# Optimization experiments

Hardware: AMD Instinct MI355X
Metric: run time of the kernel (lower is better)

## Reference

```python
import jax, jax.numpy as jnp
import numpy as np

DIM = 32
N_HOP = 2
N_MEMORY = 32
BATCH = 2048
N_ENTITY = 100000
N_RELATION = 48


def _gru_cell(x, h, w_ih, w_hh, b_ih, b_hh):
    # PyTorch GRUCell semantics
    gi = x @ w_ih.T + b_ih          # [b, 3d]
    gh = h @ w_hh.T + b_hh          # [b, 3d]
    i_r, i_z, i_n = jnp.split(gi, 3, axis=-1)
    h_r, h_z, h_n = jnp.split(gh, 3, axis=-1)
    r = jax.nn.sigmoid(i_r + h_r)
    z = jax.nn.sigmoid(i_z + h_z)
    n = jnp.tanh(i_n + r * h_n)
    return (1.0 - z) * n + z * h


def setup_inputs() -> dict:
    key = jax.random.key(0)
    ks = jax.random.split(key, 16)
    h_i = jax.random.randint(ks[0], (BATCH, N_HOP, N_MEMORY), 0, N_ENTITY)
    R_i = jax.random.randint(ks[1], (BATCH, N_HOP, N_MEMORY), 0, N_RELATION)
    t_i = jax.random.randint(ks[2], (BATCH, N_HOP, N_MEMORY), 0, N_ENTITY)
    v_i = jax.random.randint(ks[3], (BATCH,), 0, N_ENTITY)
    s = 0.05
    entity_emb = jax.random.normal(ks[4], (N_ENTITY, DIM), jnp.float32) * s
    relation_emb = jax.random.normal(ks[5], (N_RELATION, DIM, DIM), jnp.float32) * s
    agg_w1 = jax.random.normal(ks[6], (DIM, 4 * DIM), jnp.float32) * s
    agg_b1 = jnp.zeros((DIM,), jnp.float32)
    agg_w2 = jax.random.normal(ks[7], (1, DIM), jnp.float32) * s
    agg_b2 = jnp.zeros((1,), jnp.float32)
    gru_w_ih = jax.random.normal(ks[8], (N_HOP, 3 * DIM, DIM), jnp.float32) * s
    gru_w_hh = jax.random.normal(ks[9], (N_HOP, 3 * DIM, DIM), jnp.float32) * s
    gru_b_ih = jnp.zeros((N_HOP, 3 * DIM), jnp.float32)
    gru_b_hh = jnp.zeros((N_HOP, 3 * DIM), jnp.float32)
    ans_w = jax.random.normal(ks[10], (DIM, DIM), jnp.float32) * s
    ans_b = jnp.zeros((DIM,), jnp.float32)
    return {
        'h_i': h_i, 'R_i': R_i, 't_i': t_i, 'v_i': v_i,
        'entity_emb': entity_emb, 'relation_emb': relation_emb,
        'agg_w1': agg_w1, 'agg_b1': agg_b1, 'agg_w2': agg_w2, 'agg_b2': agg_b2,
        'gru_w_ih': gru_w_ih, 'gru_w_hh': gru_w_hh,
        'gru_b_ih': gru_b_ih, 'gru_b_hh': gru_b_hh,
        'ans_w': ans_w, 'ans_b': ans_b,
    }


def reference(h_i, R_i, t_i, v_i, entity_emb, relation_emb,
              agg_w1, agg_b1, agg_w2, agg_b2,
              gru_w_ih, gru_w_hh, gru_b_ih, gru_b_hh,
              ans_w, ans_b):
    # InputModule: embedding gathers
    vs = entity_emb[v_i]                     # [b, d]
    hs = entity_emb[h_i]                     # [b, H, m, d]
    ts = entity_emb[t_i]                     # [b, H, m, d]
    Rs = relation_emb[R_i]                   # [b, H, m, d, d]

    M = vs
    n_hop = hs.shape[1]
    for hop in range(n_hop):
        R = Rs[:, hop]                       # [b, m, d, d]
        h = hs[:, hop]                       # [b, m, d]
        t = ts[:, hop]                       # [b, m, d]
        Rh = jnp.einsum('bmij,bmj->bmi', R, h)   # [b, m, d]
        vexp = vs[:, None, :]
        mexp = M[:, None, :]
        z = jnp.concatenate([Rh * vexp, Rh * mexp,
                             jnp.abs(Rh - vexp), jnp.abs(Rh - mexp)], axis=2)  # [b, m, 4d]
        # AggregateFnc: tanh(Linear) -> Linear(d,1); dropout is eval-mode identity
        Z = jnp.tanh(z @ agg_w1.T + agg_b1) @ agg_w2.T + agg_b2   # [b, m, 1]
        g = jax.nn.softmax(Z[..., 0], axis=1)[..., None]           # [b, m, 1]
        o = jnp.sum(t * g, axis=1)                                 # [b, d]
        M = _gru_cell(o, M, gru_w_ih[hop], gru_w_hh[hop],
                      gru_b_ih[hop], gru_b_hh[hop])
    # AnswerModule (dropout = identity in eval)
    Mw = jax.nn.sigmoid(M @ ans_w.T + ans_b)
    return jnp.sum(vs * Mw, axis=1)          # [b]
```

## Files before the change

### kernel.cpp

```cpp
#include <hip/hip_runtime.h>
#include <hip/hip_bf16.h>


#define NHOP 2

typedef __attribute__((ext_vector_type(4)))  float f32x4;
typedef __attribute__((ext_vector_type(8)))  short bf16x8s;
typedef __attribute__((ext_vector_type(4)))  int   i32x4;

__device__ __forceinline__ float sigmoid_f(float x){ return 1.0f/(1.0f+__expf(-x)); }
__device__ __forceinline__ float tanh_f(float x){
  float e = __expf(2.0f*x);
  return 1.0f - 2.0f/(e + 1.0f);
}
__device__ __forceinline__ unsigned pk_bf16(float lo, float hi){
  __hip_bfloat162 h = __float22bfloat162_rn(make_float2(lo, hi));
  return *reinterpret_cast<unsigned*>(&h);
}
__device__ __forceinline__ float bfly8(float p[8], bool bb4, bool bb2, bool bb1){
  #pragma unroll
  for (int k = 0; k < 4; ++k){
    float send = bb4 ? p[k] : p[k+4];
    float t = __shfl_xor(send, 4);
    p[k] = (bb4 ? p[k+4] : p[k]) + t;
  }
  #pragma unroll
  for (int k = 0; k < 2; ++k){
    float send = bb2 ? p[k] : p[k+2];
    float t = __shfl_xor(send, 2);
    p[k] = (bb2 ? p[k+2] : p[k]) + t;
  }
  float send = bb1 ? p[0] : p[1];
  float t = __shfl_xor(send, 1);
  return (bb1 ? p[1] : p[0]) + t;
}

__global__ __launch_bounds__(256) void ripple_fused(
    const int* __restrict__ h_i, const int* __restrict__ R_i, const int* __restrict__ t_i,
    const int* __restrict__ v_i,
    const float* __restrict__ entity_emb, const float* __restrict__ relation_emb,
    const float* __restrict__ agg_w1, const float* __restrict__ agg_b1,
    const float* __restrict__ agg_w2, const float* __restrict__ agg_b2,
    const float* __restrict__ gru_w_ih, const float* __restrict__ gru_w_hh,
    const float* __restrict__ gru_b_ih, const float* __restrict__ gru_b_hh,
    const float* __restrict__ ans_w, const float* __restrict__ ans_b,
    float* __restrict__ out, int batch)
{
  __shared__ __align__(16) int   s_bfrag[8*64*4];
  __shared__ __align__(16) float s_rhA[2][2][32*33];
  __shared__ __align__(16) float s_vsM[2][64];
  __shared__ __align__(16) float s_zpart[2][64];
  __shared__ __align__(16) float s_opart[2][4*32];
  __shared__ __align__(16) float s_M[2][32];
  __shared__ __align__(16) float s_gig[2][192];

  const int bid = blockIdx.x;
  const int eA  = bid*2;
  const int eB  = (eA + 1 < batch) ? eA + 1 : eA;
  const int tid = threadIdx.x;
  const int g   = tid >> 5;
  const int o   = tid & 31;
  const int l   = tid & 63;
  const int w   = tid >> 6;
  const int c   = o & 7;
  const int r_  = o >> 3;
  const bool bb4 = (c & 4) != 0;
  const bool bb2 = (c & 2) != 0;
  const bool bb1 = (c & 1) != 0;

  #pragma unroll
  for (int k = 0; k < 2; ++k){
    int s  = tid + k*256;
    int f  = s >> 6, li = s & 63;
    int x  = f >> 1, otf = f & 1;
    const float* src = agg_w1 + (otf*16 + (li & 15))*128 + x*32 + ((li >> 4) & 3)*8;
    float4 f0 = *(const float4*)src;
    float4 f1 = *(const float4*)(src + 4);
    *(int4*)&s_bfrag[s*4] = make_int4((int)pk_bf16(f0.x, f0.y), (int)pk_bf16(f0.z, f0.w),
                                      (int)pk_bf16(f1.x, f1.y), (int)pk_bf16(f1.z, f1.w));
  }
  if (tid < 64){
    int e  = tid >> 5, oo = tid & 31;
    float v = entity_emb[(size_t)v_i[e ? eB : eA]*32 + oo];
    s_vsM[e][oo*2+0] = v; s_vsM[e][oo*2+1] = v; s_M[e][oo] = v;
  }

  {
    const int iA = c*4 + r_;
    const int bgm = g*4;
    int rAc = R_i[(eA*NHOP + 0)*32 + bgm];
    int hAc = h_i[(eA*NHOP + 0)*32 + bgm];
    int rBc = R_i[(eB*NHOP + 0)*32 + bgm];
    int hBc = h_i[(eB*NHOP + 0)*32 + bgm];
    #pragma unroll 1
    for (int it = 0; it < 8; ++it){
      const int hp = it >> 2;
      const int m  = bgm + (it & 3);
      int rAn = rAc, hAn = hAc, rBn = rBc, hBn = hBc;
      if (it < 7){
        const int nhp = (it + 1) >> 2;
        const int nm  = bgm + ((it + 1) & 3);
        rAn = R_i[(eA*NHOP + nhp)*32 + nm];
        hAn = h_i[(eA*NHOP + nhp)*32 + nm];
        rBn = R_i[(eB*NHOP + nhp)*32 + nm];
        hBn = h_i[(eB*NHOP + nhp)*32 + nm];
      }
      const float* RbA = relation_emb + (size_t)rAc*1024;
      const float* RbB = relation_emb + (size_t)rBc*1024;
      float4 hvA = *(const float4*)(entity_emb + (size_t)hAc*32 + c*4);
      float4 hvB = *(const float4*)(entity_emb + (size_t)hBc*32 + c*4);
      float pA[8], pB[8];
      #pragma unroll
      for (int q = 0; q < 8; ++q){
        float4 rv = *(const float4*)(RbA + q*128 + o*4);
        pA[q] = rv.x*hvA.x + rv.y*hvA.y + rv.z*hvA.z + rv.w*hvA.w;
      }
      #pragma unroll
      for (int q = 0; q < 8; ++q){
        float4 rv = *(const float4*)(RbB + q*128 + o*4);
        pB[q] = rv.x*hvB.x + rv.y*hvB.y + rv.z*hvB.z + rv.w*hvB.w;
      }
      float a0 = bfly8(pA, bb4, bb2, bb1);
      float a1 = bfly8(pB, bb4, bb2, bb1);
      s_rhA[0][hp][m*33 + iA] = a0;
      s_rhA[1][hp][m*33 + iA] = a1;
      rAc = rAn; hAc = hAn; rBc = rBn; hBc = hBn;
    }
  }
  __syncthreads();

  const int mt  = w >> 1, ot = w & 1;
  const int col = l & 15;
  const int kg  = l >> 4;
  const float b1o = agg_b1[ot*16 + col];
  const float w2o = agg_w2[ot*16 + col];
  i32x4 bv[4];
  #pragma unroll
  for (int x = 0; x < 4; ++x)
    bv[x] = *(const i32x4*)&s_bfrag[((x*2 + ot)*64 + l)*4];

  for (int hop = 0; hop < NHOP; ++hop){
    float tvA[4], tvB[4];
    #pragma unroll
    for (int ml = 0; ml < 4; ++ml){
      tvA[ml] = entity_emb[(size_t)t_i[(eA*NHOP + hop)*32 + g*4 + ml]*32 + o];
      tvB[ml] = entity_emb[(size_t)t_i[(eB*NHOP + hop)*32 + g*4 + ml]*32 + o];
    }

    {
      #pragma unroll
      for (int e = 0; e < 2; ++e){
        const float* rp = &s_rhA[e][hop][(mt*16 + col)*33 + kg*8];
        float4 q0 = *(const float4*)(rp);
        float4 q1 = *(const float4*)(rp + 4);
        float rh[8] = {q0.x,q0.y,q0.z,q0.w,q1.x,q1.y,q1.z,q1.w};
        unsigned aw[4][4];
        #pragma unroll
        for (int q = 0; q < 4; ++q){
          int i0 = kg*8 + 2*q;
          float2 vm0 = *(const float2*)&s_vsM[e][i0*2];
          float2 vm1 = *(const float2*)&s_vsM[e][(i0+1)*2];
          float e0 = rh[2*q], e1 = rh[2*q+1];
          aw[0][q] = pk_bf16(e0*vm0.x,        e1*vm1.x);
          aw[1][q] = pk_bf16(e0*vm0.y,        e1*vm1.y);
          aw[2][q] = pk_bf16(fabsf(e0-vm0.x), fabsf(e1-vm1.x));
          aw[3][q] = pk_bf16(fabsf(e0-vm0.y), fabsf(e1-vm1.y));
        }
        f32x4 acc = {0.f, 0.f, 0.f, 0.f};
        #pragma unroll
        for (int x = 0; x < 4; ++x){
          i32x4 av = {(int)aw[x][0], (int)aw[x][1], (int)aw[x][2], (int)aw[x][3]};
          acc = __builtin_amdgcn_mfma_f32_16x16x32_bf16(
                  __builtin_bit_cast(bf16x8s, av),
                  __builtin_bit_cast(bf16x8s, bv[x]), acc, 0, 0, 0);
        }
        float v[4];
        #pragma unroll
        for (int r = 0; r < 4; ++r) v[r] = tanh_f(acc[r] + b1o) * w2o;
        const bool b3 = (l & 8) != 0;
        #pragma unroll
        for (int k = 0; k < 2; ++k){
          float send = b3 ? v[k] : v[k+2];
          float tt = __shfl_xor(send, 8);
          v[k] = (b3 ? v[k+2] : v[k]) + tt;
        }
        const bool b2_ = (l & 4) != 0;
        {
          float send = b2_ ? v[0] : v[1];
          float tt = __shfl_xor(send, 4);
          v[0] = (b2_ ? v[1] : v[0]) + tt;
        }
        v[0] += __shfl_xor(v[0], 2);
        v[0] += __shfl_xor(v[0], 1);
        if ((l & 3) == 0){
          int m_local = kg*4 + ((l >> 3) & 1)*2 + ((l >> 2) & 1);
          s_zpart[e][ot*32 + mt*16 + m_local] = v[0];
        }
      }
    }
    __syncthreads();

    #pragma unroll
    for (int e = 0; e < 2; ++e){
      float z  = s_zpart[e][o] + s_zpart[e][32 + o];
      float mx = z;
      #pragma unroll
      for (int s = 16; s > 0; s >>= 1) mx = fmaxf(mx, __shfl_xor(mx, s));
      float ex = __expf(z - mx);
      float sm = ex;
      #pragma unroll
      for (int s = 16; s > 0; s >>= 1) sm += __shfl_xor(sm, s);
      float gval = ex / sm;
      float po = 0.f;
      #pragma unroll
      for (int ml = 0; ml < 4; ++ml)
        po += __shfl(gval, g*4 + ml) * (e == 0 ? tvA[ml] : tvB[ml]);
      po += __shfl_xor(po, 32);
      if (l < 32) s_opart[e][w*32 + o] = po;
    }
    __syncthreads();

    {
      const int cc = (tid & 7) * 4;
      const int rr = tid >> 3;
      float4 oA = make_float4(0,0,0,0), oB = make_float4(0,0,0,0);
      #pragma unroll
      for (int gg = 0; gg < 4; ++gg){
        float4 ta = *(const float4*)&s_opart[0][gg*32 + cc];
        float4 tb = *(const float4*)&s_opart[1][gg*32 + cc];
        oA.x += ta.x; oA.y += ta.y; oA.z += ta.z; oA.w += ta.w;
        oB.x += tb.x; oB.y += tb.y; oB.z += tb.z; oB.w += tb.w;
      }
      float4 mA = *(const float4*)&s_M[0][cc];
      float4 mB = *(const float4*)&s_M[1][cc];
      #pragma unroll
      for (int k = 0; k < 3; ++k){
        int row = k*32 + rr;
        float4 wi = *(const float4*)(gru_w_ih + ((size_t)hop*96 + row)*32 + cc);
        float4 wh = *(const float4*)(gru_w_hh + ((size_t)hop*96 + row)*32 + cc);
        float aiA = wi.x*oA.x + wi.y*oA.y + wi.z*oA.z + wi.w*oA.w;
        float ahA = wh.x*mA.x + wh.y*mA.y + wh.z*mA.z + wh.w*mA.w;
        float aiB = wi.x*oB.x + wi.y*oB.y + wi.z*oB.z + wi.w*oB.w;
        float ahB = wh.x*mB.x + wh.y*mB.y + wh.z*mB.z + wh.w*mB.w;
        aiA += __shfl_xor(aiA,1); aiA += __shfl_xor(aiA,2); aiA += __shfl_xor(aiA,4);
        ahA += __shfl_xor(ahA,1); ahA += __shfl_xor(ahA,2); ahA += __shfl_xor(ahA,4);
        aiB += __shfl_xor(aiB,1); aiB += __shfl_xor(aiB,2); aiB += __shfl_xor(aiB,4);
        ahB += __shfl_xor(ahB,1); ahB += __shfl_xor(ahB,2); ahB += __shfl_xor(ahB,4);
        if ((tid & 7) == 0){
          s_gig[0][row]      = aiA;
          s_gig[0][96 + row] = ahA;
          s_gig[1][row]      = aiB;
          s_gig[1][96 + row] = ahB;
        }
      }
    }
    __syncthreads();

    if (tid < 64){
      int e = tid >> 5, oo = tid & 31;
      const float* bih = gru_b_ih + hop*96;
      const float* bhh = gru_b_hh + hop*96;
      float ir = s_gig[e][oo]       + bih[oo];
      float iz = s_gig[e][32 + oo]  + bih[32 + oo];
      float in_= s_gig[e][64 + oo]  + bih[64 + oo];
      float hr = s_gig[e][96 + oo]  + bhh[oo];
      float hz = s_gig[e][128 + oo] + bhh[32 + oo];
      float hn = s_gig[e][160 + oo] + bhh[64 + oo];
      float r  = sigmoid_f(ir + hr);
      float zz = sigmoid_f(iz + hz);
      float n  = tanh_f(in_ + r*hn);
      float Mn = (1.f - zz)*n + zz*s_M[e][oo];
      s_M[e][oo] = Mn;
      s_vsM[e][oo*2+1] = Mn;
    }
    __syncthreads();
  }

  #pragma unroll
  for (int e = 0; e < 2; ++e){
    const int cc = (tid & 7) * 4;
    const int rr = tid >> 3;
    float4 m4 = *(const float4*)&s_M[e][cc];
    float4 aw = *(const float4*)(ans_w + (size_t)rr*32 + cc);
    float a = aw.x*m4.x + aw.y*m4.y + aw.z*m4.z + aw.w*m4.w;
    a += __shfl_xor(a,1); a += __shfl_xor(a,2); a += __shfl_xor(a,4);
    if ((tid & 7) == 0) s_zpart[e][rr] = sigmoid_f(a + ans_b[rr]);
  }
  __syncthreads();
  if (tid < 64){
    int e = tid >> 5, oo = tid & 31;
    float val = s_vsM[e][oo*2+0] * s_zpart[e][oo];
    #pragma unroll
    for (int s = 16; s > 0; s >>= 1) val += __shfl_xor(val, s);
    if (oo == 0) out[e ? eB : eA] = val;
  }
}

extern "C" void kernel_launch(void* const* d_in, const int* in_sizes, int n_in,
                              void* d_out, int out_size, void* d_ws, size_t ws_size,
                              hipStream_t stream) {
  const int*   h_i          = (const int*)  d_in[0];
  const int*   R_i          = (const int*)  d_in[1];
  const int*   t_i          = (const int*)  d_in[2];
  const int*   v_i          = (const int*)  d_in[3];
  const float* entity_emb   = (const float*)d_in[4];
  const float* relation_emb = (const float*)d_in[5];
  const float* agg_w1       = (const float*)d_in[6];
  const float* agg_b1       = (const float*)d_in[7];
  const float* agg_w2       = (const float*)d_in[8];
  const float* agg_b2       = (const float*)d_in[9];
  const float* gru_w_ih     = (const float*)d_in[10];
  const float* gru_w_hh     = (const float*)d_in[11];
  const float* gru_b_ih     = (const float*)d_in[12];
  const float* gru_b_hh     = (const float*)d_in[13];
  const float* ans_w        = (const float*)d_in[14];
  const float* ans_b        = (const float*)d_in[15];
  (void)agg_b2;
  float* outp = (float*)d_out;

  const int batch = in_sizes[3];
  const int grid  = (batch + 1) / 2;
  ripple_fused<<<grid, 256, 0, stream>>>(
      h_i, R_i, t_i, v_i, entity_emb, relation_emb,
      agg_w1, agg_b1, agg_w2, agg_b2,
      gru_w_ih, gru_w_hh, gru_b_ih, gru_b_hh,
      ans_w, ans_b, outp, batch);
}
```

Measured before the change: 40.98 us.

## Split relation-matrix GEMV into separate kernel writing to workspace

Moves the per-memory R·h product out of the fused kernel into a standalone rh_gemv kernel, where each 32-lane group computes one Rh vector and writes it to the workspace. The main kernel then loads the precomputed Rh from the workspace into shared memory instead of gathering 4KB relation matrices itself. The aim is to take the gather-heavy GEMV off the serial per-block path and spread it across many more threads. The cost is an extra launch plus a round trip of about 16MB through global memory. If the workspace is too small, the original fused kernel still runs.

```diff
diff --git a/kernel.cpp b/kernel.cpp
--- a/kernel.cpp
+++ b/kernel.cpp
@@ -33,6 +33,263 @@
   float send = bb1 ? p[0] : p[1];
   float t = __shfl_xor(send, 1);
   return (bb1 ? p[1] : p[0]) + t;
+}
+
+__global__ __launch_bounds__(256) void rh_gemv(
+    const int* __restrict__ h_i, const int* __restrict__ R_i,
+    const float* __restrict__ entity_emb, const float* __restrict__ relation_emb,
+    float* __restrict__ ws, int ntask)
+{
+  const int hw = (blockIdx.x*256 + threadIdx.x) >> 5;
+  if (hw >= ntask) return;
+  const int o  = threadIdx.x & 31;
+  const int c  = o & 7;
+  const int r_ = o >> 3;
+  const bool bb4 = (c & 4) != 0;
+  const bool bb2 = (c & 2) != 0;
+  const bool bb1 = (c & 1) != 0;
+
+  const int ridx = R_i[hw];
+  const int hidx = h_i[hw];
+  const float* Rbase = relation_emb + (size_t)ridx*1024;
+  float4 hv = *(const float4*)(entity_emb + (size_t)hidx*32 + c*4);
+  float p[8];
+  #pragma unroll
+  for (int q = 0; q < 8; ++q){
+    float4 rv = *(const float4*)(Rbase + q*128 + o*4);
+    p[q] = rv.x*hv.x + rv.y*hv.y + rv.z*hv.z + rv.w*hv.w;
+  }
+  float a = bfly8(p, bb4, bb2, bb1);
+  ws[(size_t)hw*32 + (c*4 + r_)] = a;
+}
+
+__global__ __launch_bounds__(256) void ripple_main(
+    const int* __restrict__ t_i, const int* __restrict__ v_i,
+    const float* __restrict__ entity_emb,
+    const float* __restrict__ agg_w1, const float* __restrict__ agg_b1,
+    const float* __restrict__ agg_w2,
+    const float* __restrict__ gru_w_ih, const float* __restrict__ gru_w_hh,
+    const float* __restrict__ gru_b_ih, const float* __restrict__ gru_b_hh,
+    const float* __restrict__ ans_w, const float* __restrict__ ans_b,
+    const float* __restrict__ ws,
+    float* __restrict__ out, int batch)
+{
+  __shared__ __align__(16) int   s_bfrag[8*64*4];
+  __shared__ __align__(16) float s_rhA[2][2][32*33];
+  __shared__ __align__(16) float s_vsM[2][64];
+  __shared__ __align__(16) float s_zpart[2][64];
+  __shared__ __align__(16) float s_opart[2][4*32];
+  __shared__ __align__(16) float s_M[2][32];
+  __shared__ __align__(16) float s_gig[2][192];
+
+  const int bid = blockIdx.x;
+  const int eA  = bid*2;
+  const int eB  = (eA + 1 < batch) ? eA + 1 : eA;
+  const int tid = threadIdx.x;
+  const int g   = tid >> 5;
+  const int o   = tid & 31;
+  const int l   = tid & 63;
+  const int w   = tid >> 6;
+
+  #pragma unroll
+  for (int k = 0; k < 2; ++k){
+    int s  = tid + k*256;
+    int f  = s >> 6, li = s & 63;
+    int x  = f >> 1, otf = f & 1;
+    const float* src = agg_w1 + (otf*16 + (li & 15))*128 + x*32 + ((li >> 4) & 3)*8;
+    float4 f0 = *(const float4*)src;
+    float4 f1 = *(const float4*)(src + 4);
+    *(int4*)&s_bfrag[s*4] = make_int4((int)pk_bf16(f0.x, f0.y), (int)pk_bf16(f0.z, f0.w),
+                                      (int)pk_bf16(f1.x, f1.y), (int)pk_bf16(f1.z, f1.w));
+  }
+  if (tid < 64){
+    int e  = tid >> 5, oo = tid & 31;
+    float v = entity_emb[(size_t)v_i[e ? eB : eA]*32 + oo];
+    s_vsM[e][oo*2+0] = v; s_vsM[e][oo*2+1] = v; s_M[e][oo] = v;
+  }
+
+  {
+    const float4* wsA = (const float4*)(ws + (size_t)eA*NHOP*32*32);
+    const float4* wsB = (const float4*)(ws + (size_t)eB*NHOP*32*32);
+    #pragma unroll
+    for (int k = 0; k < 2; ++k){
+      int f    = tid + k*256;
+      int task = f >> 3;
+      int i4   = f & 7;
+      int hp   = task >> 5, m = task & 31;
+      float4 va = wsA[f];
+      float4 vb = wsB[f];
+      *(float4*)&s_rhA[0][hp][m*33 + i4*4] = va;
+      *(float4*)&s_rhA[1][hp][m*33 + i4*4] = vb;
+    }
+  }
+  __syncthreads();
+
+  const int mt  = w >> 1, ot = w & 1;
+  const int col = l & 15;
+  const int kg  = l >> 4;
+  const float b1o = agg_b1[ot*16 + col];
+  const float w2o = agg_w2[ot*16 + col];
+  i32x4 bv[4];
+  #pragma unroll
+  for (int x = 0; x < 4; ++x)
+    bv[x] = *(const i32x4*)&s_bfrag[((x*2 + ot)*64 + l)*4];
+
+  for (int hop = 0; hop < NHOP; ++hop){
+    float tvA[4], tvB[4];
+    #pragma unroll
+    for (int ml = 0; ml < 4; ++ml){
+      tvA[ml] = entity_emb[(size_t)t_i[(eA*NHOP + hop)*32 + g*4 + ml]*32 + o];
+      tvB[ml] = entity_emb[(size_t)t_i[(eB*NHOP + hop)*32 + g*4 + ml]*32 + o];
+    }
+
+    {
+      #pragma unroll
+      for (int e = 0; e < 2; ++e){
+        const float* rp = &s_rhA[e][hop][(mt*16 + col)*33 + kg*8];
+        float4 q0 = *(const float4*)(rp);
+        float4 q1 = *(const float4*)(rp + 4);
+        float rh[8] = {q0.x,q0.y,q0.z,q0.w,q1.x,q1.y,q1.z,q1.w};
+        unsigned aw[4][4];
+        #pragma unroll
+        for (int q = 0; q < 4; ++q){
+          int i0 = kg*8 + 2*q;
+          float2 vm0 = *(const float2*)&s_vsM[e][i0*2];
+          float2 vm1 = *(const float2*)&s_vsM[e][(i0+1)*2];
+          float e0 = rh[2*q], e1 = rh[2*q+1];
+          aw[0][q] = pk_bf16(e0*vm0.x,        e1*vm1.x);
+          aw[1][q] = pk_bf16(e0*vm0.y,        e1*vm1.y);
+          aw[2][q] = pk_bf16(fabsf(e0-vm0.x), fabsf(e1-vm1.x));
+          aw[3][q] = pk_bf16(fabsf(e0-vm0.y), fabsf(e1-vm1.y));
+        }
+        f32x4 acc = {0.f, 0.f, 0.f, 0.f};
+        #pragma unroll
+        for (int x = 0; x < 4; ++x){
+          i32x4 av = {(int)aw[x][0], (int)aw[x][1], (int)aw[x][2], (int)aw[x][3]};
+          acc = __builtin_amdgcn_mfma_f32_16x16x32_bf16(
+                  __builtin_bit_cast(bf16x8s, av),
+                  __builtin_bit_cast(bf16x8s, bv[x]), acc, 0, 0, 0);
+        }
+        float v[4];
+        #pragma unroll
+        for (int r = 0; r < 4; ++r) v[r] = tanh_f(acc[r] + b1o) * w2o;
+        const bool b3 = (l & 8) != 0;
+        #pragma unroll
+        for (int k = 0; k < 2; ++k){
+          float send = b3 ? v[k] : v[k+2];
+          float tt = __shfl_xor(send, 8);
+          v[k] = (b3 ? v[k+2] : v[k]) + tt;
+        }
+        const bool b2_ = (l & 4) != 0;
+        {
+          float send = b2_ ? v[0] : v[1];
+          float tt = __shfl_xor(send, 4);
+          v[0] = (b2_ ? v[1] : v[0]) + tt;
+        }
+        v[0] += __shfl_xor(v[0], 2);
+        v[0] += __shfl_xor(v[0], 1);
+        if ((l & 3) == 0){
+          int m_local = kg*4 + ((l >> 3) & 1)*2 + ((l >> 2) & 1);
+          s_zpart[e][ot*32 + mt*16 + m_local] = v[0];
+        }
+      }
+    }
+    __syncthreads();
+
+    #pragma unroll
+    for (int e = 0; e < 2; ++e){
+      float z  = s_zpart[e][o] + s_zpart[e][32 + o];
+      float mx = z;
+      #pragma unroll
+      for (int s = 16; s > 0; s >>= 1) mx = fmaxf(mx, __shfl_xor(mx, s));
+      float ex = __expf(z - mx);
+      float sm = ex;
+      #pragma unroll
+      for (int s = 16; s > 0; s >>= 1) sm += __shfl_xor(sm, s);
+      float gval = ex / sm;
+      float po = 0.f;
+      #pragma unroll
+      for (int ml = 0; ml < 4; ++ml)
+        po += __shfl(gval, g*4 + ml) * (e == 0 ? tvA[ml] : tvB[ml]);
+      po += __shfl_xor(po, 32);
+      if (l < 32) s_opart[e][w*32 + o] = po;
+    }
+    __syncthreads();
+
+    {
+      const int cc = (tid & 7) * 4;
+      const int rr = tid >> 3;
+      float4 oA = make_float4(0,0,0,0), oB = make_float4(0,0,0,0);
+      #pragma unroll
+      for (int gg = 0; gg < 4; ++gg){
+        float4 ta = *(const float4*)&s_opart[0][gg*32 + cc];
+        float4 tb = *(const float4*)&s_opart[1][gg*32 + cc];
+        oA.x += ta.x; oA.y += ta.y; oA.z += ta.z; oA.w += ta.w;
+        oB.x += tb.x; oB.y += tb.y; oB.z += tb.z; oB.w += tb.w;
+      }
+      float4 mA = *(const float4*)&s_M[0][cc];
+      float4 mB = *(const float4*)&s_M[1][cc];
+      #pragma unroll
+      for (int k = 0; k < 3; ++k){
+        int row = k*32 + rr;
+        float4 wi = *(const float4*)(gru_w_ih + ((size_t)hop*96 + row)*32 + cc);
+        float4 wh = *(const float4*)(gru_w_hh + ((size_t)hop*96 + row)*32 + cc);
+        float aiA = wi.x*oA.x + wi.y*oA.y + wi.z*oA.z + wi.w*oA.w;
+        float ahA = wh.x*mA.x + wh.y*mA.y + wh.z*mA.z + wh.w*mA.w;
+        float aiB = wi.x*oB.x + wi.y*oB.y + wi.z*oB.z + wi.w*oB.w;
+        float ahB = wh.x*mB.x + wh.y*mB.y + wh.z*mB.z + wh.w*mB.w;
+        aiA += __shfl_xor(aiA,1); aiA += __shfl_xor(aiA,2); aiA += __shfl_xor(aiA,4);
+        ahA += __shfl_xor(ahA,1); ahA += __shfl_xor(ahA,2); ahA += __shfl_xor(ahA,4);
+        aiB += __shfl_xor(aiB,1); aiB += __shfl_xor(aiB,2); aiB += __shfl_xor(aiB,4);
+        ahB += __shfl_xor(ahB,1); ahB += __shfl_xor(ahB,2); ahB += __shfl_xor(ahB,4);
+        if ((tid & 7) == 0){
+          s_gig[0][row]      = aiA;
+          s_gig[0][96 + row] = ahA;
+          s_gig[1][row]      = aiB;
+          s_gig[1][96 + row] = ahB;
+        }
+      }
+    }
+    __syncthreads();
+
+    if (tid < 64){
+      int e = tid >> 5, oo = tid & 31;
+      const float* bih = gru_b_ih + hop*96;
+      const float* bhh = gru_b_hh + hop*96;
+      float ir = s_gig[e][oo]       + bih[oo];
+      float iz = s_gig[e][32 + oo]  + bih[32 + oo];
+      float in_= s_gig[e][64 + oo]  + bih[64 + oo];
+      float hr = s_gig[e][96 + oo]  + bhh[oo];
+      float hz = s_gig[e][128 + oo] + bhh[32 + oo];
+      float hn = s_gig[e][160 + oo] + bhh[64 + oo];
+      float r  = sigmoid_f(ir + hr);
+      float zz = sigmoid_f(iz + hz);
+      float n  = tanh_f(in_ + r*hn);
+      float Mn = (1.f - zz)*n + zz*s_M[e][oo];
+      s_M[e][oo] = Mn;
+      s_vsM[e][oo*2+1] = Mn;
+    }
+    __syncthreads();
+  }
+
+  #pragma unroll
+  for (int e = 0; e < 2; ++e){
+    const int cc = (tid & 7) * 4;
+    const int rr = tid >> 3;
+    float4 m4 = *(const float4*)&s_M[e][cc];
+    float4 aw = *(const float4*)(ans_w + (size_t)rr*32 + cc);
+    float a = aw.x*m4.x + aw.y*m4.y + aw.z*m4.z + aw.w*m4.w;
+    a += __shfl_xor(a,1); a += __shfl_xor(a,2); a += __shfl_xor(a,4);
+    if ((tid & 7) == 0) s_zpart[e][rr] = sigmoid_f(a + ans_b[rr]);
+  }
+  __syncthreads();
+  if (tid < 64){
+    int e = tid >> 5, oo = tid & 31;
+    float val = s_vsM[e][oo*2+0] * s_zpart[e][oo];
+    #pragma unroll
+    for (int s = 16; s > 0; s >>= 1) val += __shfl_xor(val, s);
+    if (oo == 0) out[e ? eB : eA] = val;
+  }
 }
 
 __global__ __launch_bounds__(256) void ripple_fused(
@@ -40,7 +297,7 @@
     const int* __restrict__ v_i,
     const float* __restrict__ entity_emb, const float* __restrict__ relation_emb,
     const float* __restrict__ agg_w1, const float* __restrict__ agg_b1,
-    const float* __restrict__ agg_w2, const float* __restrict__ agg_b2,
+    const float* __restrict__ agg_w2,
     const float* __restrict__ gru_w_ih, const float* __restrict__ gru_w_hh,
     const float* __restrict__ gru_b_ih, const float* __restrict__ gru_b_hh,
     const float* __restrict__ ans_w, const float* __restrict__ ans_b,
@@ -84,7 +341,6 @@
     float v = entity_emb[(size_t)v_i[e ? eB : eA]*32 + oo];
     s_vsM[e][oo*2+0] = v; s_vsM[e][oo*2+1] = v; s_M[e][oo] = v;
   }
-
   {
     const int iA = c*4 + r_;
     const int bgm = g*4;
@@ -146,7 +402,6 @@
       tvA[ml] = entity_emb[(size_t)t_i[(eA*NHOP + hop)*32 + g*4 + ml]*32 + o];
       tvB[ml] = entity_emb[(size_t)t_i[(eB*NHOP + hop)*32 + g*4 + ml]*32 + o];
     }
-
     {
       #pragma unroll
       for (int e = 0; e < 2; ++e){
@@ -199,7 +454,6 @@
       }
     }
     __syncthreads();
-
     #pragma unroll
     for (int e = 0; e < 2; ++e){
       float z  = s_zpart[e][o] + s_zpart[e][32 + o];
@@ -219,7 +473,6 @@
       if (l < 32) s_opart[e][w*32 + o] = po;
     }
     __syncthreads();
-
     {
       const int cc = (tid & 7) * 4;
       const int rr = tid >> 3;
@@ -255,7 +508,6 @@
       }
     }
     __syncthreads();
-
     if (tid < 64){
       int e = tid >> 5, oo = tid & 31;
       const float* bih = gru_b_ih + hop*96;
@@ -275,7 +527,6 @@
     }
     __syncthreads();
   }
-
   #pragma unroll
   for (int e = 0; e < 2; ++e){
     const int cc = (tid & 7) * 4;
@@ -308,21 +559,31 @@
   const float* agg_w1       = (const float*)d_in[6];
   const float* agg_b1       = (const float*)d_in[7];
   const float* agg_w2       = (const float*)d_in[8];
-  const float* agg_b2       = (const float*)d_in[9];
   const float* gru_w_ih     = (const float*)d_in[10];
   const float* gru_w_hh     = (const float*)d_in[11];
   const float* gru_b_ih     = (const float*)d_in[12];
   const float* gru_b_hh     = (const float*)d_in[13];
   const float* ans_w        = (const float*)d_in[14];
   const float* ans_b        = (const float*)d_in[15];
-  (void)agg_b2;
   float* outp = (float*)d_out;
 
   const int batch = in_sizes[3];
-  const int grid  = (batch + 1) / 2;
-  ripple_fused<<<grid, 256, 0, stream>>>(
-      h_i, R_i, t_i, v_i, entity_emb, relation_emb,
-      agg_w1, agg_b1, agg_w2, agg_b2,
-      gru_w_ih, gru_w_hh, gru_b_ih, gru_b_hh,
-      ans_w, ans_b, outp, batch);
-}
+  const int ntask = batch * NHOP * 32;
+  const size_t need = (size_t)ntask * 32 * sizeof(float);
+
+  if (ws_size >= need) {
+    float* ws = (float*)d_ws;
+    rh_gemv<<<(ntask + 7) / 8, 256, 0, stream>>>(
+        h_i, R_i, entity_emb, relation_emb, ws, ntask);
+    ripple_main<<<(batch + 1) / 2, 256, 0, stream>>>(
+        t_i, v_i, entity_emb, agg_w1, agg_b1, agg_w2,
+        gru_w_ih, gru_w_hh, gru_b_ih, gru_b_hh,
+        ans_w, ans_b, ws, outp, batch);
+  } else {
+    ripple_fused<<<(batch + 1) / 2, 256, 0, stream>>>(
+        h_i, R_i, t_i, v_i, entity_emb, relation_emb,
+        agg_w1, agg_b1, agg_w2,
+        gru_w_ih, gru_w_hh, gru_b_ih, gru_b_hh,
+        ans_w, ans_b, outp, batch);
+  }
+}
```

New measurement: 51.26 us. 1.25x slower.
